# Kernel optimization log

Hardware: AMD Instinct MI355X
Metric: run time of the kernel (lower is better)

The kernel has to match this reference:

```python
import jax, jax.numpy as jnp
import numpy as np

N = 100000
E = 800000
D_IN = 64
D_HID = 64
D_OUT = 47


def gcn_conv(x, edge_index, W, b):
    # GCNConv with normalize=False: linear transform then sum-aggregate over edges.
    h = x @ W                              # [N, d_out]
    src, dst = edge_index[0], edge_index[1]
    msg = h[src]                           # [E, d_out] gather
    agg = jax.ops.segment_sum(msg, dst, num_segments=N)  # [N, d_out] scatter-add
    return agg + b


def setup_inputs() -> dict:
    key = jax.random.key(0)
    ks = jax.random.split(key, 8)
    x = jax.random.normal(ks[0], (N, D_IN), dtype=jnp.float32)
    edge_index = jax.random.randint(ks[1], (2, E), 0, N, dtype=jnp.int64)
    # Glorot-ish init for weights, zeros for bias (as in GCNConv.reset_parameters)
    def glorot(k, fan_in, fan_out):
        s = jnp.sqrt(6.0 / (fan_in + fan_out))
        return jax.random.uniform(k, (fan_in, fan_out), jnp.float32, -s, s)
    W1 = glorot(ks[2], D_IN, D_HID)
    b1 = jnp.zeros((D_HID,), jnp.float32)
    W2 = glorot(ks[3], D_HID, D_HID)
    b2 = jnp.zeros((D_HID,), jnp.float32)
    W3 = glorot(ks[4], D_HID, D_OUT)
    b3 = jnp.zeros((D_OUT,), jnp.float32)
    return {"x": x, "edge_index": edge_index,
            "W1": W1, "b1": b1, "W2": W2, "b2": b2, "W3": W3, "b3": b3}


def reference(x, edge_index, W1, b1, W2, b2, W3, b3):
    # Layer 1: conv -> relu (dropout is identity at inference)
    h = jax.nn.relu(gcn_conv(x, edge_index, W1, b1))
    # Layer 2
    h = jax.nn.relu(gcn_conv(h, edge_index, W2, b2))
    # Output layer + log_softmax over classes
    out = gcn_conv(h, edge_index, W3, b3)
    return jax.nn.log_softmax(out, axis=-1)
```

## Files before the change

kernel.cpp:

```cpp
#include <hip/hip_runtime.h>
#include <cmath>


#define B1_EPB 4096
#define BKT_SH 8
#define CHUNK  256
#define PSTRIDE 512

typedef __attribute__((ext_vector_type(8))) short bf8;
typedef __attribute__((ext_vector_type(4))) float f4;

__device__ __forceinline__ unsigned int f2bf(float x) {
  unsigned int u = __float_as_uint(x);
  return (u + 0x7FFFu + ((u >> 16) & 1u)) >> 16;
}
__device__ __forceinline__ float bflo(unsigned int u) { return __uint_as_float(u << 16); }
__device__ __forceinline__ float bfhi(unsigned int u) { return __uint_as_float(u & 0xFFFF0000u); }

__global__ void bhist_cvt_k(const int* __restrict__ dsti, int* __restrict__ part,
                            int ne, const float* __restrict__ x,
                            unsigned short* __restrict__ xb, int n4,
                            int nbkt, int nseg) {
  __shared__ int lh[PSTRIDE];
  const int b = blockIdx.x, t = threadIdx.x;
  if (b < nseg) {
    for (int i = t; i < PSTRIDE; i += 256) lh[i] = 0;
    __syncthreads();
    const int base = b * B1_EPB;
    const int m = min(B1_EPB, ne - base);
    for (int i = t; i < m; i += 256) atomicAdd(&lh[dsti[base + i] >> BKT_SH], 1);
    __syncthreads();
    for (int i = t; i < PSTRIDE; i += 256) part[b * PSTRIDE + i] = lh[i];
  }
  const int gid = b * 256 + t, gst = gridDim.x * 256;
  for (int j = gid; j < n4; j += gst) {
    float4 v = ((const float4*)x)[j];
    ushort4 o;
    o.x = (unsigned short)f2bf(v.x); o.y = (unsigned short)f2bf(v.y);
    o.z = (unsigned short)f2bf(v.z); o.w = (unsigned short)f2bf(v.w);
    ((ushort4*)xb)[j] = o;
  }
}

__global__ void btot_k(const int* __restrict__ part, int* __restrict__ btot,
                       int nseg) {
  __shared__ int sh[256];
  const int t = threadIdx.x;
  const int bkt = (blockIdx.x << 6) + (t & 63);
  int s0 = 0, s1 = 0, s2 = 0, s3 = 0, s4 = 0, s5 = 0, s6 = 0, s7 = 0;
  int seg = t >> 6;
  for (; seg + 28 < nseg; seg += 32) {
    s0 += part[(seg +  0) * PSTRIDE + bkt];
    s1 += part[(seg +  4) * PSTRIDE + bkt];
    s2 += part[(seg +  8) * PSTRIDE + bkt];
    s3 += part[(seg + 12) * PSTRIDE + bkt];
    s4 += part[(seg + 16) * PSTRIDE + bkt];
    s5 += part[(seg + 20) * PSTRIDE + bkt];
    s6 += part[(seg + 24) * PSTRIDE + bkt];
    s7 += part[(seg + 28) * PSTRIDE + bkt];
  }
  for (; seg < nseg; seg += 4) s0 += part[seg * PSTRIDE + bkt];
  sh[t] = ((s0 + s1) + (s2 + s3)) + ((s4 + s5) + (s6 + s7));
  __syncthreads();
  if (t < 64) btot[bkt] = sh[t] + sh[t + 64] + sh[t + 128] + sh[t + 192];
}

__global__ void bscan_k(const int* __restrict__ btot, int* __restrict__ bbase,
                        int* __restrict__ bcur, int nbkt, int ne) {
  __shared__ int sh[512];
  const int t = threadIdx.x;
  const int s = btot[t];
  sh[t] = s; __syncthreads();
  for (int o = 1; o < 512; o <<= 1) {
    int v = (t >= o) ? sh[t - o] : 0; __syncthreads();
    sh[t] += v; __syncthreads();
  }
  if (t < nbkt) { int e = sh[t] - s; bbase[t] = e; bcur[t] = e; }
  if (t == 0) bbase[nbkt] = ne;
}

__global__ void bucket_k(const int* __restrict__ srci, const int* __restrict__ dsti,
                         const int* __restrict__ part, int* __restrict__ bcur,
                         uint2* __restrict__ ebuf, int ne, int nbkt) {
  __shared__ int lcur[512], lbase[512];
  const int t = threadIdx.x;
  const int base = blockIdx.x * B1_EPB;
  const int m = min(B1_EPB, ne - base);
  for (int i = t; i < nbkt; i += 256) {
    const int c = part[blockIdx.x * PSTRIDE + i];
    lbase[i] = c ? atomicAdd(&bcur[i], c) : 0;
    lcur[i] = 0;
  }
  __syncthreads();
  for (int i = t; i < m; i += 256) {
    const int s = srci[base + i], d = dsti[base + i];
    const int b = d >> BKT_SH;
    const int p = lbase[b] + atomicAdd(&lcur[b], 1);
    ebuf[p] = make_uint2((unsigned)s, (unsigned)d);
  }
}

__global__ void fillb_k(const uint2* __restrict__ ebuf, const int* __restrict__ bbase,
                        int* __restrict__ row_off, int* __restrict__ ssrc,
                        int n, int ne) {
  __shared__ int lcnt[256], lpre[256], lcur[256];
  const int b = blockIdx.x, t = threadIdx.x;
  const int v0 = b << BKT_SH;
  const int nv = min(1 << BKT_SH, n - v0);
  const int start = bbase[b], end = bbase[b + 1];
  lcnt[t] = 0; __syncthreads();
  for (int i = start + t; i < end; i += 256)
    atomicAdd(&lcnt[ebuf[i].y & ((1 << BKT_SH) - 1)], 1);
  __syncthreads();
  const int x = lcnt[t];
  lpre[t] = x; __syncthreads();
  for (int o = 1; o < 256; o <<= 1) {
    int v = (t >= o) ? lpre[t - o] : 0; __syncthreads();
    lpre[t] += v; __syncthreads();
  }
  const int excl = start + lpre[t] - x;
  lcur[t] = excl;
  if (t < nv) row_off[v0 + t] = excl;
  if (t == 0) row_off[v0 + nv] = end;
  __syncthreads();
  for (int i = start + t; i < end; i += 256) {
    const uint2 e = ebuf[i];
    const int p = atomicAdd(&lcur[e.y & ((1 << BKT_SH) - 1)], 1);
    ssrc[p] = (int)e.x;
  }
}

template <int DOUT, bool LS>
__launch_bounds__(256, 4)
__global__ void fused_k(const unsigned short* __restrict__ in,
                        const int* __restrict__ row_off, const int* __restrict__ ssrc,
                        const float* __restrict__ Wm, const float* __restrict__ bin,
                        void* __restrict__ outp, int n) {
  constexpr int NT = (DOUT + 15) / 16;
  const int lane  = threadIdx.x & 63;
  const int wslot = threadIdx.x >> 6;
  const int quad  = lane >> 4;
  const int f16i  = lane & 15;
  const int hw    = (f16i >> 3) & 1;
  const int j8    = f16i & 7;

  __shared__ char rows_raw[4][16 * 144];
  __shared__ int  sidx[4][CHUNK];
  __shared__ unsigned short Wt[64 * 72];
  char* my  = rows_raw[wslot];
  int*  sid = sidx[wslot];

  {
    const int t = threadIdx.x;
    for (int i = t; i < 64 * 72; i += 256) Wt[i] = 0;
    __syncthreads();
    for (int i = t; i < 64 * DOUT; i += 256) {
      const int k = i / DOUT, c = i - k * DOUT;
      Wt[c * 72 + k] = (unsigned short)f2bf(Wm[i]);
    }
  }
  float bc[NT];
#pragma unroll
  for (int t = 0; t < NT; ++t) {
    const int c = t * 16 + f16i;
    bc[t] = (c < DOUT) ? bin[c] : 0.f;
  }
  __syncthreads();

  const uint4* in4 = (const uint4*)in;
  const int wid = (int)((blockIdx.x * blockDim.x + threadIdx.x) >> 6);
  const int nwv = (int)((gridDim.x * blockDim.x) >> 6);
  const int ntiles = (n + 15) >> 4;

  for (int tile = wid; tile < ntiles; tile += nwv) {
    const int v0 = tile << 4;
    const int ro_l = row_off[min(v0 + min(lane, 16), n)];
    const int base     = __shfl(ro_l, 0, 64);
    const int tile_end = __shfl(ro_l, 16, 64);
    int ns[4], nE[4];
#pragma unroll
    for (int r = 0; r < 4; ++r) {
      const int m = quad * 4 + r;
      ns[r] = __shfl(ro_l, m, 64);
      nE[r] = __shfl(ro_l, m + 1, 64);
    }

    float acc[4][8];
#pragma unroll
    for (int r = 0; r < 4; ++r)
#pragma unroll
      for (int i = 0; i < 8; ++i) acc[r][i] = 0.f;

    for (int off = base; off < tile_end; off += CHUNK) {
      const int cend = min(tile_end, off + CHUNK);
      const int nL = cend - off;
#pragma unroll
      for (int k = 0; k < CHUNK / 64; ++k) {
        const int p = off + lane + k * 64;
        if (p < cend) sid[lane + k * 64] = ssrc[p];
      }
      asm volatile("s_waitcnt lgkmcnt(0)" ::: "memory");

#pragma unroll
      for (int r = 0; r < 4; ++r) {
        const int ls = max(ns[r], off), le = min(nE[r], cend);
        for (int c = ls; c < le; c += 16) {
          uint4 q[8];
#pragma unroll
          for (int k = 0; k < 8; ++k) {
            const int e = c + (k << 1) + hw;
            const int lofs = min(e - off, nL - 1);
            const int s = sid[lofs];
            q[k] = (e < le) ? in4[(size_t)s * 8 + j8]
                            : make_uint4(0u, 0u, 0u, 0u);
          }
#pragma unroll
          for (int k = 0; k < 8; ++k) {
            acc[r][0] += bflo(q[k].x); acc[r][1] += bfhi(q[k].x);
            acc[r][2] += bflo(q[k].y); acc[r][3] += bfhi(q[k].y);
            acc[r][4] += bflo(q[k].z); acc[r][5] += bfhi(q[k].z);
            acc[r][6] += bflo(q[k].w); acc[r][7] += bfhi(q[k].w);
          }
        }
      }
    }

#pragma unroll
    for (int r = 0; r < 4; ++r) {
#pragma unroll
      for (int i = 0; i < 8; ++i) acc[r][i] += __shfl_xor(acc[r][i], 8, 64);
      if (hw == 0) {
        const int m = quad * 4 + r;
        uint4 p;
        p.x = f2bf(acc[r][0]) | (f2bf(acc[r][1]) << 16);
        p.y = f2bf(acc[r][2]) | (f2bf(acc[r][3]) << 16);
        p.z = f2bf(acc[r][4]) | (f2bf(acc[r][5]) << 16);
        p.w = f2bf(acc[r][6]) | (f2bf(acc[r][7]) << 16);
        *(uint4*)(my + m * 144 + j8 * 16) = p;
      }
    }
    asm volatile("s_waitcnt lgkmcnt(0)" ::: "memory");

    bf8 a0 = *(const bf8*)(my + f16i * 144 + quad * 16);
    bf8 a1 = *(const bf8*)(my + f16i * 144 + quad * 16 + 64);
    f4 acc2[NT];
#pragma unroll
    for (int t = 0; t < NT; ++t) {
      const unsigned short* wp = Wt + (t * 16 + f16i) * 72 + quad * 8;
      bf8 w0 = *(const bf8*)(wp);
      bf8 w1 = *(const bf8*)(wp + 32);
      f4 z = {0.f, 0.f, 0.f, 0.f};
      acc2[t] = __builtin_amdgcn_mfma_f32_16x16x32_bf16(a0, w0, z, 0, 0, 0);
      acc2[t] = __builtin_amdgcn_mfma_f32_16x16x32_bf16(a1, w1, acc2[t], 0, 0, 0);
    }

    if (!LS) {
      unsigned short* ob = (unsigned short*)outp;
#pragma unroll
      for (int t = 0; t < NT; ++t)
#pragma unroll
        for (int j = 0; j < 4; ++j) {
          const int v = v0 + quad * 4 + j;
          if (v < n) {
            float val = acc2[t][j] + bc[t];
            ob[(size_t)v * 64 + t * 16 + f16i] =
                (unsigned short)f2bf(fmaxf(val, 0.f));
          }
        }
    } else {
      float* ob = (float*)outp;
      float val[NT][4];
#pragma unroll
      for (int t = 0; t < NT; ++t)
#pragma unroll
        for (int j = 0; j < 4; ++j) val[t][j] = acc2[t][j] + bc[t];
#pragma unroll
      for (int j = 0; j < 4; ++j) {
        float mx = -INFINITY;
#pragma unroll
        for (int t = 0; t < NT; ++t)
          if (t * 16 + f16i < DOUT) mx = fmaxf(mx, val[t][j]);
#pragma unroll
        for (int o = 1; o <= 8; o <<= 1) mx = fmaxf(mx, __shfl_xor(mx, o, 64));
        float sm = 0.f;
#pragma unroll
        for (int t = 0; t < NT; ++t)
          if (t * 16 + f16i < DOUT) sm += __expf(val[t][j] - mx);
#pragma unroll
        for (int o = 1; o <= 8; o <<= 1) sm += __shfl_xor(sm, o, 64);
        const float lse = mx + __logf(sm);
        const int v = v0 + quad * 4 + j;
        if (v < n) {
#pragma unroll
          for (int t = 0; t < NT; ++t) {
            const int c = t * 16 + f16i;
            if (c < DOUT) ob[(size_t)v * DOUT + c] = val[t][j] - lse;
          }
        }
      }
    }
  }
}

extern "C" void kernel_launch(void* const* d_in, const int* in_sizes, int n_in,
                              void* d_out, int out_size, void* d_ws, size_t ws_size,
                              hipStream_t stream) {
  const float* x  = (const float*)d_in[0];
  const int*   ei = (const int*)d_in[1];
  const float* W1 = (const float*)d_in[2];
  const float* b1 = (const float*)d_in[3];
  const float* W2 = (const float*)d_in[4];
  const float* b2 = (const float*)d_in[5];
  const float* W3 = (const float*)d_in[6];
  const float* b3 = (const float*)d_in[7];
  float* outp = (float*)d_out;

  const int n  = in_sizes[0] / 64;
  const int ne = in_sizes[1] / 2;
  const int* srci = ei;
  const int* dsti = ei + ne;
  const int nbkt = (n + (1 << BKT_SH) - 1) >> BKT_SH;
  const int nseg = (ne + B1_EPB - 1) / B1_EPB;

  const size_t N64 = (size_t)n * 64;
  unsigned short* xb   = (unsigned short*)d_ws;
  unsigned short* bufA = xb + N64;
  unsigned short* bufB = bufA + N64;
  uint2* ebuf   = (uint2*)(bufB + N64);
  int* row_off  = (int*)(ebuf + ne);
  int* part     = row_off + n + 1;
  int* bbase    = part + nseg * PSTRIDE;
  int* bcur     = bbase + nbkt + 1;
  int* btot     = bcur + nbkt;
  int* ssrc     = btot + 512;

  const int TB = 256;
  const int fus_blocks = 1568;

  bhist_cvt_k<<<784, TB, 0, stream>>>(dsti, part, ne, x, xb, (int)(N64 / 4), nbkt, nseg);
  btot_k<<<8, TB, 0, stream>>>(part, btot, nseg);
  bscan_k<<<1, 512, 0, stream>>>(btot, bbase, bcur, nbkt, ne);
  bucket_k<<<nseg, TB, 0, stream>>>(srci, dsti, part, bcur, ebuf, ne, nbkt);
  fillb_k<<<nbkt, TB, 0, stream>>>(ebuf, bbase, row_off, ssrc, n, ne);

  fused_k<64, false><<<fus_blocks, TB, 0, stream>>>(xb,   row_off, ssrc, W1, b1, bufA, n);
  fused_k<64, false><<<fus_blocks, TB, 0, stream>>>(bufA, row_off, ssrc, W2, b2, bufB, n);
  fused_k<47, true ><<<fus_blocks, TB, 0, stream>>>(bufB, row_off, ssrc, W3, b3, outp, n);
}
```

Measured before the change: 207.0 us.

## Merge bucket totals into scan, prefetch next tile indices, halve fused grid

The bucket-total kernel is folded into the single-block scan kernel, which now sums the per-segment histograms itself, removing one launch. In the fused GCN kernel, each wave prefetches the next tile's row offsets and its first chunk of source indices into shared memory during the epilogue of the current tile, so that load latency overlaps the transform work. The fused grid is halved, so each wave handles more tiles and gets more benefit from the prefetch. Risks: the single-block scan now does about 196 serial reads per thread, and fewer blocks reduce the latency hiding available for the gather.

```diff
diff --git a/kernel.cpp b/kernel.cpp
--- a/kernel.cpp
+++ b/kernel.cpp
@@ -42,34 +42,24 @@
   }
 }
 
-__global__ void btot_k(const int* __restrict__ part, int* __restrict__ btot,
-                       int nseg) {
-  __shared__ int sh[256];
-  const int t = threadIdx.x;
-  const int bkt = (blockIdx.x << 6) + (t & 63);
-  int s0 = 0, s1 = 0, s2 = 0, s3 = 0, s4 = 0, s5 = 0, s6 = 0, s7 = 0;
-  int seg = t >> 6;
-  for (; seg + 28 < nseg; seg += 32) {
-    s0 += part[(seg +  0) * PSTRIDE + bkt];
-    s1 += part[(seg +  4) * PSTRIDE + bkt];
-    s2 += part[(seg +  8) * PSTRIDE + bkt];
-    s3 += part[(seg + 12) * PSTRIDE + bkt];
-    s4 += part[(seg + 16) * PSTRIDE + bkt];
-    s5 += part[(seg + 20) * PSTRIDE + bkt];
-    s6 += part[(seg + 24) * PSTRIDE + bkt];
-    s7 += part[(seg + 28) * PSTRIDE + bkt];
-  }
-  for (; seg < nseg; seg += 4) s0 += part[seg * PSTRIDE + bkt];
-  sh[t] = ((s0 + s1) + (s2 + s3)) + ((s4 + s5) + (s6 + s7));
-  __syncthreads();
-  if (t < 64) btot[bkt] = sh[t] + sh[t + 64] + sh[t + 128] + sh[t + 192];
-}
-
-__global__ void bscan_k(const int* __restrict__ btot, int* __restrict__ bbase,
-                        int* __restrict__ bcur, int nbkt, int ne) {
+__global__ void bscan_k(const int* __restrict__ part, int* __restrict__ bbase,
+                        int* __restrict__ bcur, int nbkt, int nseg, int ne) {
   __shared__ int sh[512];
   const int t = threadIdx.x;
-  const int s = btot[t];
+  int s0 = 0, s1 = 0, s2 = 0, s3 = 0, s4 = 0, s5 = 0, s6 = 0, s7 = 0;
+  int b = 0;
+  for (; b + 7 < nseg; b += 8) {
+    s0 += part[(b + 0) * PSTRIDE + t];
+    s1 += part[(b + 1) * PSTRIDE + t];
+    s2 += part[(b + 2) * PSTRIDE + t];
+    s3 += part[(b + 3) * PSTRIDE + t];
+    s4 += part[(b + 4) * PSTRIDE + t];
+    s5 += part[(b + 5) * PSTRIDE + t];
+    s6 += part[(b + 6) * PSTRIDE + t];
+    s7 += part[(b + 7) * PSTRIDE + t];
+  }
+  for (; b < nseg; ++b) s0 += part[b * PSTRIDE + t];
+  const int s = ((s0 + s1) + (s2 + s3)) + ((s4 + s5) + (s6 + s7));
   sh[t] = s; __syncthreads();
   for (int o = 1; o < 512; o <<= 1) {
     int v = (t >= o) ? sh[t - o] : 0; __syncthreads();
@@ -172,9 +162,17 @@
   const int nwv = (int)((gridDim.x * blockDim.x) >> 6);
   const int ntiles = (n + 15) >> 4;
 
+  bool have_pref = false;
+  int ro_l = (wid < ntiles)
+                 ? row_off[min((wid << 4) + min(lane, 16), n)] : 0;
+
   for (int tile = wid; tile < ntiles; tile += nwv) {
+    const int tnext = tile + nwv;
+    int ro_next = 0;
+    if (tnext < ntiles)
+      ro_next = row_off[min((tnext << 4) + min(lane, 16), n)];
+
     const int v0 = tile << 4;
-    const int ro_l = row_off[min(v0 + min(lane, 16), n)];
     const int base     = __shfl(ro_l, 0, 64);
     const int tile_end = __shfl(ro_l, 16, 64);
     int ns[4], nE[4];
@@ -194,10 +192,12 @@
     for (int off = base; off < tile_end; off += CHUNK) {
       const int cend = min(tile_end, off + CHUNK);
       const int nL = cend - off;
-#pragma unroll
-      for (int k = 0; k < CHUNK / 64; ++k) {
-        const int p = off + lane + k * 64;
-        if (p < cend) sid[lane + k * 64] = ssrc[p];
+      if (!(have_pref && off == base)) {
+#pragma unroll
+        for (int k = 0; k < CHUNK / 64; ++k) {
+          const int p = off + lane + k * 64;
+          if (p < cend) sid[lane + k * 64] = ssrc[p];
+        }
       }
       asm volatile("s_waitcnt lgkmcnt(0)" ::: "memory");
 
@@ -223,6 +223,19 @@
           }
         }
       }
+    }
+
+    bool pref_ok = false;
+    if (tnext < ntiles) {
+      const int base_n = __shfl(ro_next, 0, 64);
+      const int tend_n = __shfl(ro_next, 16, 64);
+      const int cend_n = min(tend_n, base_n + CHUNK);
+#pragma unroll
+      for (int k = 0; k < CHUNK / 64; ++k) {
+        const int p = base_n + lane + k * 64;
+        if (p < cend_n) sid[lane + k * 64] = ssrc[p];
+      }
+      pref_ok = true;
     }
 
 #pragma unroll
@@ -299,6 +312,9 @@
         }
       }
     }
+
+    have_pref = pref_ok;
+    ro_l = ro_next;
   }
 }
 
@@ -331,15 +347,13 @@
   int* part     = row_off + n + 1;
   int* bbase    = part + nseg * PSTRIDE;
   int* bcur     = bbase + nbkt + 1;
-  int* btot     = bcur + nbkt;
-  int* ssrc     = btot + 512;
+  int* ssrc     = bcur + nbkt;
 
   const int TB = 256;
-  const int fus_blocks = 1568;
+  const int fus_blocks = 784;
 
   bhist_cvt_k<<<784, TB, 0, stream>>>(dsti, part, ne, x, xb, (int)(N64 / 4), nbkt, nseg);
-  btot_k<<<8, TB, 0, stream>>>(part, btot, nseg);
-  bscan_k<<<1, 512, 0, stream>>>(btot, bbase, bcur, nbkt, ne);
+  bscan_k<<<1, 512, 0, stream>>>(part, bbase, bcur, nbkt, nseg, ne);
   bucket_k<<<nseg, TB, 0, stream>>>(srci, dsti, part, bcur, ebuf, ne, nbkt);
   fillb_k<<<nbkt, TB, 0, stream>>>(ebuf, bbase, row_off, ssrc, n, ne);
 
```

After: 208.2 us. No clear change (+0.6%).
